# Optimization experiments

Hardware: AMD Instinct MI355X
Metric: run time of the kernel (lower is better)

Reference implementation:

```python
import jax, jax.numpy as jnp
import numpy as np

N, E, D = 50000, 1600000, 128


def _mk_w(key, shape):
    return jax.random.normal(key, shape, dtype=jnp.float32) * 0.05


def setup_inputs() -> dict:
    key = jax.random.key(0)
    ks = jax.random.split(key, 32)
    inp = {
        'x_in': jax.random.normal(ks[0], (N, D), dtype=jnp.float32),
        'rows': jax.random.randint(ks[1], (E,), 0, N, dtype=jnp.int64 if jax.config.jax_enable_x64 else jnp.int32),
        'cols': jax.random.randint(ks[2], (E,), 0, N, dtype=jnp.int64 if jax.config.jax_enable_x64 else jnp.int32),
        'vals': jax.random.uniform(ks[3], (E,), dtype=jnp.float32),
    }
    names = ['m1_W1', 'm1_W2', 'm2_W1', 'm2_W2', 'Wu1', 'Wu2', 'Wr1', 'Wr2', 'Wo1', 'Wo2']
    for i, n in enumerate(names):
        inp[n] = _mk_w(ks[4 + i], (D, D))
        inp[n.replace('W', 'b')] = jnp.zeros((D,), dtype=jnp.float32)
    return inp


def _mlp2(x, W1, b1, W2, b2):
    # 2-layer MLP: Linear -> ReLU -> Linear
    return jax.nn.relu(x @ W1 + b1) @ W2 + b2


def reference(x_in, rows, cols, vals,
              m1_W1, m1_b1, m1_W2, m1_b2,
              m2_W1, m2_b1, m2_W2, m2_b2,
              Wu1, bu1, Wu2, bu2,
              Wr1, br1, Wr2, br2,
              Wo1, bo1, Wo2, bo2):
    x = _mlp2(x_in, m1_W1, m1_b1, m1_W2, m1_b2)            # [N, D]
    # sparse COO spmm: out[i] = sum_e vals[e] * x[cols[e]] for rows[e] == i
    msgs = vals[:, None] * x[cols]                          # [E, D]
    agg = jax.ops.segment_sum(msgs, rows, num_segments=N)   # [N, D]
    out = _mlp2(agg, m2_W1, m2_b1, m2_W2, m2_b2)
    z = jax.nn.sigmoid(out @ Wu1 + bu1 + x @ Wu2 + bu2)
    r = jax.nn.sigmoid(out @ Wr1 + br1 + x @ Wr2 + br2)
    h = jnp.tanh(out @ Wo1 + bo1 + (r * x) @ Wo2 + bo2)
    return (1.0 - z) * x + z * h
```

## Files before the change

### kernel.cpp

```cpp
#include <hip/hip_runtime.h>

#define DD 128
#define BSHIFT 7
#define BROWS 128
#define MS_TILE 4096
#define MS_EPT 8
#define STAGE_CAP 6144

typedef __attribute__((ext_vector_type(8))) short short8;
typedef __attribute__((ext_vector_type(4))) float f32x4;
typedef unsigned short u16;
typedef unsigned int u32;

__device__ __forceinline__ u16 f2bf(float f) {
  u32 u = __builtin_bit_cast(u32, f);
  u += 0x7fffu + ((u >> 16) & 1u);
  return (u16)(u >> 16);
}
__device__ __forceinline__ float bf2f(u16 s) {
  u32 u = ((u32)s) << 16;
  return __builtin_bit_cast(float, u);
}
__device__ __forceinline__ float f16val(u32 cv) {
  return (float)__builtin_bit_cast(_Float16, (u16)(cv & 0xffffu));
}
__device__ __forceinline__ float sigmoidf_(float v) { return 1.f / (1.f + __expf(-v)); }
__device__ __forceinline__ float tanhf_(float v) {
  float e = __expf(-2.f * v);
  return (1.f - e) / (1.f + e);
}

struct WPtrs { const float* w[10]; };

__global__ void pack_weights(WPtrs wp, u16* __restrict__ bp) {
  const float* W = wp.w[blockIdx.x];
  u16* out = bp + (size_t)blockIdx.x * 16384;
  for (int o = threadIdx.x; o < 16384; o += blockDim.x) {
    int e = o & 7, lane = (o >> 3) & 63, nt = (o >> 9) & 7, ks = o >> 12;
    int k = ks * 32 + (lane >> 4) * 8 + e;
    int c = (lane & 15) + nt * 16;
    out[o] = f2bf(W[k * DD + c]);
  }
}

__global__ __launch_bounds__(512) void multisplit(const int* __restrict__ rows,
                                                  const int* __restrict__ cols,
                                                  const float* __restrict__ vals,
                                                  int* __restrict__ cursor,
                                                  uint2* __restrict__ recs,
                                                  int E, int NB, int cap) {
  __shared__ u32 hist[512];
  __shared__ u32 scan_tmp[512];
  __shared__ u32 hbase[512];
  __shared__ int gbase[512];
  __shared__ u32 rankc[512];
  __shared__ uint2 stage[MS_TILE];
  const int t = threadIdx.x;
  const int tile0 = blockIdx.x * MS_TILE;
  hist[t] = 0;
  rankc[t] = 0;
  __syncthreads();
  int myb[MS_EPT];
  u32 mycv[MS_EPT], myrow[MS_EPT];
#pragma unroll
  for (int j = 0; j < MS_EPT; ++j) {
    int e = tile0 + j * 512 + t;
    if (e < E) {
      int r = rows[e];
      int b = r >> BSHIFT;
      myb[j] = b;
      myrow[j] = (u32)r;
      _Float16 hf = (_Float16)vals[e];
      mycv[j] = ((u32)cols[e] << 16) | (u32)__builtin_bit_cast(u16, hf);
      atomicAdd(&hist[b], 1u);
    } else {
      myb[j] = -1;
    }
  }
  __syncthreads();
  u32 v = hist[t];
  scan_tmp[t] = v;
  __syncthreads();
  for (int o = 1; o < 512; o <<= 1) {
    u32 x = (t >= o) ? scan_tmp[t - o] : 0;
    __syncthreads();
    scan_tmp[t] += x;
    __syncthreads();
  }
  hbase[t] = scan_tmp[t] - v;
  if (t < NB && v > 0) gbase[t] = atomicAdd(&cursor[t], (int)v);
  __syncthreads();
#pragma unroll
  for (int j = 0; j < MS_EPT; ++j) {
    if (myb[j] >= 0) {
      u32 rk = atomicAdd(&rankc[myb[j]], 1u);
      stage[hbase[myb[j]] + rk].x = mycv[j];
      stage[hbase[myb[j]] + rk].y = myrow[j];
    }
  }
  __syncthreads();
  int cnt = E - tile0;
  cnt = cnt < MS_TILE ? cnt : MS_TILE;
  for (int k = t; k < cnt; k += 512) {
    uint2 rec = stage[k];
    int b = (int)(rec.y >> BSHIFT);
    int off = gbase[b] + (k - (int)hbase[b]);
    if (off < cap) recs[(size_t)b * cap + off] = rec;
  }
}

__global__ __launch_bounds__(512) void bucket_csr(const uint2* __restrict__ recs,
                                                  const int* __restrict__ cursor,
                                                  u32* __restrict__ recs2,
                                                  int* __restrict__ rowstart,
                                                  int* __restrict__ rowcnt, int n, int cap) {
  __shared__ int hist[BROWS];
  __shared__ int sc[BROWS];
  __shared__ int hbase[BROWS];
  __shared__ u32 rank[BROWS];
  __shared__ u32 stage[STAGE_CAP];
  const int t = threadIdx.x;
  const int b = blockIdx.x;
  int cnt = cursor[b];
  cnt = cnt < cap ? cnt : cap;
  const uint2* rb = recs + (size_t)b * cap;
  if (t < BROWS) { hist[t] = 0; rank[t] = 0; }
  __syncthreads();
  for (int i = t; i < cnt; i += 512) atomicAdd(&hist[rb[i].y & (BROWS - 1)], 1);
  __syncthreads();
  if (t < BROWS) sc[t] = hist[t];
  __syncthreads();
  for (int o = 1; o < BROWS; o <<= 1) {
    int x = (t >= o && t < BROWS) ? sc[t - o] : 0;
    __syncthreads();
    if (t < BROWS) sc[t] += x;
    __syncthreads();
  }
  if (t < BROWS) {
    hbase[t] = sc[t] - hist[t];
    int r = (b << BSHIFT) + t;
    if (r < n) {
      rowstart[r] = b * cap + hbase[t];
      rowcnt[r] = hist[t];
    }
  }
  __syncthreads();
  for (int i = t; i < cnt; i += 512) {
    uint2 rec = rb[i];
    int lr = (int)(rec.y & (BROWS - 1));
    u32 p = atomicAdd(&rank[lr], 1u);
    stage[hbase[lr] + p] = rec.x;
  }
  __syncthreads();
  u32* ob = recs2 + (size_t)b * cap;
  for (int i = t; i < cnt; i += 512) ob[i] = stage[i];
}

__global__ void spmm_agg(const int* __restrict__ rowstart, const int* __restrict__ rowcnt,
                         const u32* __restrict__ recs2, const u16* __restrict__ xb,
                         u16* __restrict__ aggb, int n) {
  int row = blockIdx.x * 4 + (threadIdx.x >> 6);
  int lane = threadIdx.x & 63;
  if (row >= n) return;
  int s = rowstart[row];
  int e2 = s + rowcnt[row];
  float a0 = 0.f, a1 = 0.f;
  int j = s;
  for (; j + 3 < e2; j += 4) {
    u32 pk0 = recs2[j], pk1 = recs2[j + 1], pk2 = recs2[j + 2], pk3 = recs2[j + 3];
    u32 x0 = *reinterpret_cast<const u32*>(xb + (size_t)(pk0 >> 16) * DD + lane * 2);
    u32 x1 = *reinterpret_cast<const u32*>(xb + (size_t)(pk1 >> 16) * DD + lane * 2);
    u32 x2 = *reinterpret_cast<const u32*>(xb + (size_t)(pk2 >> 16) * DD + lane * 2);
    u32 x3 = *reinterpret_cast<const u32*>(xb + (size_t)(pk3 >> 16) * DD + lane * 2);
    float v0 = f16val(pk0), v1 = f16val(pk1), v2 = f16val(pk2), v3 = f16val(pk3);
    a0 += v0 * bf2f((u16)(x0 & 0xffff)) + v1 * bf2f((u16)(x1 & 0xffff)) +
          v2 * bf2f((u16)(x2 & 0xffff)) + v3 * bf2f((u16)(x3 & 0xffff));
    a1 += v0 * bf2f((u16)(x0 >> 16)) + v1 * bf2f((u16)(x1 >> 16)) +
          v2 * bf2f((u16)(x2 >> 16)) + v3 * bf2f((u16)(x3 >> 16));
  }
  for (; j < e2; ++j) {
    u32 pk = recs2[j];
    u32 x0 = *reinterpret_cast<const u32*>(xb + (size_t)(pk >> 16) * DD + lane * 2);
    float v0 = f16val(pk);
    a0 += v0 * bf2f((u16)(x0 & 0xffff));
    a1 += v0 * bf2f((u16)(x0 >> 16));
  }
  u32 o = ((u32)f2bf(a1) << 16) | (u32)f2bf(a0);
  *reinterpret_cast<u32*>(aggb + (size_t)row * DD + lane * 2) = o;
}

template <int ASRC>
__global__ __launch_bounds__(256) void mlp_fused(const void* __restrict__ Ain,
                                                 const u16* __restrict__ W1p,
                                                 const float* __restrict__ b1,
                                                 const u16* __restrict__ W2p,
                                                 const float* __restrict__ b2,
                                                 u16* __restrict__ outB, int n) {
  __shared__ u16 sm[4][32][136];
  const int lane = threadIdx.x & 63;
  const int wid = threadIdx.x >> 6;
  const int row0 = blockIdx.x * 128 + wid * 32;
  const int ar = lane & 15, ak = (lane >> 4) * 8;
  const int crow = 4 * (lane >> 4), ccol = lane & 15;

  f32x4 acc[2][8];
#pragma unroll
  for (int m = 0; m < 2; ++m)
#pragma unroll
    for (int t = 0; t < 8; ++t) acc[m][t] = f32x4{0.f, 0.f, 0.f, 0.f};

#pragma unroll
  for (int ks = 0; ks < 4; ++ks) {
    short8 a[2];
#pragma unroll
    for (int m = 0; m < 2; ++m) {
      int r = row0 + m * 16 + ar;
      r = r < n ? r : n - 1;
      if (ASRC == 0) {
        const float* Ap = (const float*)Ain + (size_t)r * DD + ks * 32 + ak;
        float4 f0 = *reinterpret_cast<const float4*>(Ap);
        float4 f1 = *reinterpret_cast<const float4*>(Ap + 4);
        short8 tv;
        tv[0] = (short)f2bf(f0.x); tv[1] = (short)f2bf(f0.y);
        tv[2] = (short)f2bf(f0.z); tv[3] = (short)f2bf(f0.w);
        tv[4] = (short)f2bf(f1.x); tv[5] = (short)f2bf(f1.y);
        tv[6] = (short)f2bf(f1.z); tv[7] = (short)f2bf(f1.w);
        a[m] = tv;
      } else {
        a[m] = *reinterpret_cast<const short8*>((const u16*)Ain + (size_t)r * DD + ks * 32 + ak);
      }
    }
#pragma unroll
    for (int nt = 0; nt < 8; ++nt) {
      short8 bfr = *reinterpret_cast<const short8*>(W1p + (((ks * 8 + nt) * 64 + lane) * 8));
#pragma unroll
      for (int m = 0; m < 2; ++m)
        acc[m][nt] = __builtin_amdgcn_mfma_f32_16x16x32_bf16(a[m], bfr, acc[m][nt], 0, 0, 0);
    }
  }
#pragma unroll
  for (int m = 0; m < 2; ++m)
#pragma unroll
    for (int nt = 0; nt < 8; ++nt) {
      float bsv = b1[ccol + nt * 16];
#pragma unroll
      for (int e = 0; e < 4; ++e) {
        float v = acc[m][nt][e] + bsv;
        v = v > 0.f ? v : 0.f;
        sm[wid][m * 16 + crow + e][ccol + nt * 16] = f2bf(v);
      }
    }
  __syncthreads();

  f32x4 acc2[2][8];
#pragma unroll
  for (int m = 0; m < 2; ++m)
#pragma unroll
    for (int t = 0; t < 8; ++t) acc2[m][t] = f32x4{0.f, 0.f, 0.f, 0.f};
#pragma unroll
  for (int ks = 0; ks < 4; ++ks) {
    short8 a2[2];
#pragma unroll
    for (int m = 0; m < 2; ++m)
      a2[m] = *reinterpret_cast<const short8*>(&sm[wid][m * 16 + ar][ks * 32 + ak]);
#pragma unroll
    for (int nt = 0; nt < 8; ++nt) {
      short8 bfr = *reinterpret_cast<const short8*>(W2p + (((ks * 8 + nt) * 64 + lane) * 8));
#pragma unroll
      for (int m = 0; m < 2; ++m)
        acc2[m][nt] = __builtin_amdgcn_mfma_f32_16x16x32_bf16(a2[m], bfr, acc2[m][nt], 0, 0, 0);
    }
  }
#pragma unroll
  for (int m = 0; m < 2; ++m)
#pragma unroll
    for (int nt = 0; nt < 8; ++nt) {
      int col = ccol + nt * 16;
      float bsv = b2[col];
#pragma unroll
      for (int e = 0; e < 4; ++e) {
        int r = row0 + m * 16 + crow + e;
        if (r < n) outB[(size_t)r * DD + col] = f2bf(acc2[m][nt][e] + bsv);
      }
    }
}

__global__ __launch_bounds__(256) void gates_final(
    const u16* __restrict__ Ao, const u16* __restrict__ Ax, const u16* __restrict__ Wu1p,
    const u16* __restrict__ Wu2p, const u16* __restrict__ Wr1p, const u16* __restrict__ Wr2p,
    const u16* __restrict__ Wo1p, const u16* __restrict__ Wo2p, const float* __restrict__ bu1,
    const float* __restrict__ bu2, const float* __restrict__ br1, const float* __restrict__ br2,
    const float* __restrict__ bo1, const float* __restrict__ bo2, float* __restrict__ out,
    int n) {
  __shared__ u16 sm[4][16][136];
  const int lane = threadIdx.x & 63;
  const int wid = threadIdx.x >> 6;
  const int row0 = blockIdx.x * 64 + wid * 16;
  const int ar = lane & 15, ak = (lane >> 4) * 8;
  const int crow = 4 * (lane >> 4), ccol = lane & 15;

  f32x4 aZ[8], aR[8], aO[8];
#pragma unroll
  for (int t = 0; t < 8; ++t) {
    aZ[t] = f32x4{0.f, 0.f, 0.f, 0.f};
    aR[t] = f32x4{0.f, 0.f, 0.f, 0.f};
    aO[t] = f32x4{0.f, 0.f, 0.f, 0.f};
  }
#pragma unroll
  for (int ks = 0; ks < 4; ++ks) {
    int r = row0 + ar;
    r = r < n ? r : n - 1;
    short8 ao = *reinterpret_cast<const short8*>(Ao + (size_t)r * DD + ks * 32 + ak);
    short8 ax = *reinterpret_cast<const short8*>(Ax + (size_t)r * DD + ks * 32 + ak);
#pragma unroll
    for (int nt = 0; nt < 8; ++nt) {
      size_t bo = (size_t)(((ks * 8 + nt) * 64 + lane) * 8);
      short8 b1 = *reinterpret_cast<const short8*>(Wu1p + bo);
      short8 b2 = *reinterpret_cast<const short8*>(Wu2p + bo);
      short8 b3 = *reinterpret_cast<const short8*>(Wr1p + bo);
      short8 b4 = *reinterpret_cast<const short8*>(Wr2p + bo);
      short8 b5 = *reinterpret_cast<const short8*>(Wo1p + bo);
      aZ[nt] = __builtin_amdgcn_mfma_f32_16x16x32_bf16(ao, b1, aZ[nt], 0, 0, 0);
      aZ[nt] = __builtin_amdgcn_mfma_f32_16x16x32_bf16(ax, b2, aZ[nt], 0, 0, 0);
      aR[nt] = __builtin_amdgcn_mfma_f32_16x16x32_bf16(ao, b3, aR[nt], 0, 0, 0);
      aR[nt] = __builtin_amdgcn_mfma_f32_16x16x32_bf16(ax, b4, aR[nt], 0, 0, 0);
      aO[nt] = __builtin_amdgcn_mfma_f32_16x16x32_bf16(ao, b5, aO[nt], 0, 0, 0);
    }
  }
#pragma unroll
  for (int nt = 0; nt < 8; ++nt) {
    int col = ccol + nt * 16;
    float bz = bu1[col] + bu2[col];
    float br_ = br1[col] + br2[col];
    float bo_ = bo1[col];
#pragma unroll
    for (int e = 0; e < 4; ++e) {
      int r = row0 + crow + e;
      float z = sigmoidf_(aZ[nt][e] + bz);
      float rr = sigmoidf_(aR[nt][e] + br_);
      aZ[nt][e] = z;
      aO[nt][e] = aO[nt][e] + bo_;
      float xv = 0.f;
      if (r < n) xv = bf2f(Ax[(size_t)r * DD + col]);
      sm[wid][crow + e][col] = f2bf(rr * xv);
    }
  }
  __syncthreads();

  f32x4 acc2[8];
#pragma unroll
  for (int t = 0; t < 8; ++t) acc2[t] = f32x4{0.f, 0.f, 0.f, 0.f};
#pragma unroll
  for (int ks = 0; ks < 4; ++ks) {
    short8 a2 = *reinterpret_cast<const short8*>(&sm[wid][ar][ks * 32 + ak]);
#pragma unroll
    for (int nt = 0; nt < 8; ++nt) {
      short8 bfr = *reinterpret_cast<const short8*>(Wo2p + (((ks * 8 + nt) * 64 + lane) * 8));
      acc2[nt] = __builtin_amdgcn_mfma_f32_16x16x32_bf16(a2, bfr, acc2[nt], 0, 0, 0);
    }
  }
#pragma unroll
  for (int nt = 0; nt < 8; ++nt) {
    int col = ccol + nt * 16;
    float bo2v = bo2[col];
#pragma unroll
    for (int e = 0; e < 4; ++e) {
      int r = row0 + crow + e;
      if (r < n) {
        size_t idx = (size_t)r * DD + col;
        float oi = acc2[nt][e] + bo2v + aO[nt][e];
        float h = tanhf_(oi);
        float z = aZ[nt][e];
        float xv = bf2f(Ax[idx]);
        out[idx] = (1.f - z) * xv + z * h;
      }
    }
  }
}

extern "C" void kernel_launch(void* const* d_in, const int* in_sizes, int n_in,
                              void* d_out, int out_size, void* d_ws, size_t ws_size,
                              hipStream_t stream) {
  const int n = in_sizes[0] / DD;
  const int E = in_sizes[1];
  const float* x_in = (const float*)d_in[0];
  const int* rows = (const int*)d_in[1];
  const int* cols = (const int*)d_in[2];
  const float* vals = (const float*)d_in[3];
  const float* Wm[10];
  const float* Bm[10];
  for (int i = 0; i < 10; ++i) {
    Wm[i] = (const float*)d_in[4 + 2 * i];
    Bm[i] = (const float*)d_in[5 + 2 * i];
  }

  const int NB = (n + BROWS - 1) >> BSHIFT;
  int cap = (((E / NB) * 5) / 4 + 511) & ~511;
  cap = cap < STAGE_CAP ? cap : STAGE_CAP;

  char* base = (char*)d_ws;
  size_t off = 0;
  auto alloc = [&](size_t bytes) -> char* {
    char* p = base + off;
    off += (bytes + 255) & ~(size_t)255;
    return p;
  };
  u16* wpack = (u16*)alloc((size_t)10 * 16384 * 2);
  u16* x_b = (u16*)alloc((size_t)n * DD * 2);
  u16* agg_b = (u16*)alloc((size_t)n * DD * 2);
  int* cursor = (int*)alloc((size_t)NB * 4);
  int* rowstart = (int*)alloc((size_t)n * 4);
  int* rowcnt = (int*)alloc((size_t)n * 4);
  uint2* recs = (uint2*)alloc((size_t)NB * cap * 8);
  u32* recs2 = (u32*)alloc((size_t)NB * cap * 4);
  (void)ws_size;
  (void)n_in;
  (void)out_size;

  hipMemsetAsync(cursor, 0, (size_t)NB * 4, stream);
  WPtrs wp;
  for (int i = 0; i < 10; ++i) wp.w[i] = Wm[i];
  pack_weights<<<10, 256, 0, stream>>>(wp, wpack);
  multisplit<<<(E + MS_TILE - 1) / MS_TILE, 512, 0, stream>>>(rows, cols, vals, cursor, recs, E,
                                                             NB, cap);
  bucket_csr<<<NB, 512, 0, stream>>>(recs, cursor, recs2, rowstart, rowcnt, n, cap);
  int gblocks = (n + 127) / 128;
  mlp_fused<0><<<gblocks, 256, 0, stream>>>(x_in, wpack + 0 * 16384, Bm[0], wpack + 1 * 16384,
                                            Bm[1], x_b, n);
  spmm_agg<<<(n + 3) / 4, 256, 0, stream>>>(rowstart, rowcnt, recs2, x_b, agg_b, n);
  mlp_fused<1><<<gblocks, 256, 0, stream>>>(agg_b, wpack + 2 * 16384, Bm[2], wpack + 3 * 16384,
                                            Bm[3], agg_b, n);
  gates_final<<<(n + 63) / 64, 256, 0, stream>>>(
      agg_b, x_b, wpack + 4 * 16384, wpack + 5 * 16384, wpack + 6 * 16384, wpack + 7 * 16384,
      wpack + 8 * 16384, wpack + 9 * 16384, Bm[4], Bm[5], Bm[6], Bm[7], Bm[8], Bm[9],
      (float*)d_out, n);
}
```

Measured before the change: 357.1 us.

## Split MLP and gate GEMM tiles across waves by row and column halves

Result: faster. 306.1 us (-14.3%).

```diff
diff --git a/kernel.cpp b/kernel.cpp
--- a/kernel.cpp
+++ b/kernel.cpp
@@ -196,93 +196,79 @@
                                                  const u16* __restrict__ W2p,
                                                  const float* __restrict__ b2,
                                                  u16* __restrict__ outB, int n) {
-  __shared__ u16 sm[4][32][136];
+  __shared__ u16 sm[32][136];
   const int lane = threadIdx.x & 63;
   const int wid = threadIdx.x >> 6;
-  const int row0 = blockIdx.x * 128 + wid * 32;
+  const int m = wid >> 1, c = wid & 1;
+  const int row0 = blockIdx.x * 32 + m * 16;
   const int ar = lane & 15, ak = (lane >> 4) * 8;
   const int crow = 4 * (lane >> 4), ccol = lane & 15;
 
-  f32x4 acc[2][8];
-#pragma unroll
-  for (int m = 0; m < 2; ++m)
-#pragma unroll
-    for (int t = 0; t < 8; ++t) acc[m][t] = f32x4{0.f, 0.f, 0.f, 0.f};
+  f32x4 acc[4];
+#pragma unroll
+  for (int t = 0; t < 4; ++t) acc[t] = f32x4{0.f, 0.f, 0.f, 0.f};
 
 #pragma unroll
   for (int ks = 0; ks < 4; ++ks) {
-    short8 a[2];
-#pragma unroll
-    for (int m = 0; m < 2; ++m) {
-      int r = row0 + m * 16 + ar;
-      r = r < n ? r : n - 1;
-      if (ASRC == 0) {
-        const float* Ap = (const float*)Ain + (size_t)r * DD + ks * 32 + ak;
-        float4 f0 = *reinterpret_cast<const float4*>(Ap);
-        float4 f1 = *reinterpret_cast<const float4*>(Ap + 4);
-        short8 tv;
-        tv[0] = (short)f2bf(f0.x); tv[1] = (short)f2bf(f0.y);
-        tv[2] = (short)f2bf(f0.z); tv[3] = (short)f2bf(f0.w);
-        tv[4] = (short)f2bf(f1.x); tv[5] = (short)f2bf(f1.y);
-        tv[6] = (short)f2bf(f1.z); tv[7] = (short)f2bf(f1.w);
-        a[m] = tv;
-      } else {
-        a[m] = *reinterpret_cast<const short8*>((const u16*)Ain + (size_t)r * DD + ks * 32 + ak);
-      }
-    }
-#pragma unroll
-    for (int nt = 0; nt < 8; ++nt) {
+    short8 a;
+    int r = row0 + ar;
+    r = r < n ? r : n - 1;
+    if (ASRC == 0) {
+      const float* Ap = (const float*)Ain + (size_t)r * DD + ks * 32 + ak;
+      float4 f0 = *reinterpret_cast<const float4*>(Ap);
+      float4 f1 = *reinterpret_cast<const float4*>(Ap + 4);
+      short8 tv;
+      tv[0] = (short)f2bf(f0.x); tv[1] = (short)f2bf(f0.y);
+      tv[2] = (short)f2bf(f0.z); tv[3] = (short)f2bf(f0.w);
+      tv[4] = (short)f2bf(f1.x); tv[5] = (short)f2bf(f1.y);
+      tv[6] = (short)f2bf(f1.z); tv[7] = (short)f2bf(f1.w);
+      a = tv;
+    } else {
+      a = *reinterpret_cast<const short8*>((const u16*)Ain + (size_t)r * DD + ks * 32 + ak);
+    }
+#pragma unroll
+    for (int nt4 = 0; nt4 < 4; ++nt4) {
+      int nt = c * 4 + nt4;
       short8 bfr = *reinterpret_cast<const short8*>(W1p + (((ks * 8 + nt) * 64 + lane) * 8));
-#pragma unroll
-      for (int m = 0; m < 2; ++m)
-        acc[m][nt] = __builtin_amdgcn_mfma_f32_16x16x32_bf16(a[m], bfr, acc[m][nt], 0, 0, 0);
-    }
-  }
-#pragma unroll
-  for (int m = 0; m < 2; ++m)
-#pragma unroll
-    for (int nt = 0; nt < 8; ++nt) {
-      float bsv = b1[ccol + nt * 16];
-#pragma unroll
-      for (int e = 0; e < 4; ++e) {
-        float v = acc[m][nt][e] + bsv;
-        v = v > 0.f ? v : 0.f;
-        sm[wid][m * 16 + crow + e][ccol + nt * 16] = f2bf(v);
-      }
-    }
-  __syncthreads();
-
-  f32x4 acc2[2][8];
-#pragma unroll
-  for (int m = 0; m < 2; ++m)
-#pragma unroll
-    for (int t = 0; t < 8; ++t) acc2[m][t] = f32x4{0.f, 0.f, 0.f, 0.f};
+      acc[nt4] = __builtin_amdgcn_mfma_f32_16x16x32_bf16(a, bfr, acc[nt4], 0, 0, 0);
+    }
+  }
+#pragma unroll
+  for (int nt4 = 0; nt4 < 4; ++nt4) {
+    int col = (c * 4 + nt4) * 16 + ccol;
+    float bsv = b1[col];
+#pragma unroll
+    for (int e = 0; e < 4; ++e) {
+      float v = acc[nt4][e] + bsv;
+      v = v > 0.f ? v : 0.f;
+      sm[m * 16 + crow + e][col] = f2bf(v);
+    }
+  }
+  __syncthreads();
+
+  f32x4 acc2[4];
+#pragma unroll
+  for (int t = 0; t < 4; ++t) acc2[t] = f32x4{0.f, 0.f, 0.f, 0.f};
 #pragma unroll
   for (int ks = 0; ks < 4; ++ks) {
-    short8 a2[2];
-#pragma unroll
-    for (int m = 0; m < 2; ++m)
-      a2[m] = *reinterpret_cast<const short8*>(&sm[wid][m * 16 + ar][ks * 32 + ak]);
-#pragma unroll
-    for (int nt = 0; nt < 8; ++nt) {
+    short8 a2 = *reinterpret_cast<const short8*>(&sm[m * 16 + ar][ks * 32 + ak]);
+#pragma unroll
+    for (int nt4 = 0; nt4 < 4; ++nt4) {
+      int nt = c * 4 + nt4;
       short8 bfr = *reinterpret_cast<const short8*>(W2p + (((ks * 8 + nt) * 64 + lane) * 8));
-#pragma unroll
-      for (int m = 0; m < 2; ++m)
-        acc2[m][nt] = __builtin_amdgcn_mfma_f32_16x16x32_bf16(a2[m], bfr, acc2[m][nt], 0, 0, 0);
-    }
-  }
-#pragma unroll
-  for (int m = 0; m < 2; ++m)
-#pragma unroll
-    for (int nt = 0; nt < 8; ++nt) {
-      int col = ccol + nt * 16;
-      float bsv = b2[col];
-#pragma unroll
-      for (int e = 0; e < 4; ++e) {
-        int r = row0 + m * 16 + crow + e;
-        if (r < n) outB[(size_t)r * DD + col] = f2bf(acc2[m][nt][e] + bsv);
-      }
-    }
+      acc2[nt4] = __builtin_amdgcn_mfma_f32_16x16x32_bf16(a2, bfr, acc2[nt4], 0, 0, 0);
+    }
+  }
+#pragma unroll
+  for (int nt4 = 0; nt4 < 4; ++nt4) {
+    int col = (c * 4 + nt4) * 16 + ccol;
+    float bsv = b2[col];
+#pragma unroll
+    for (int e = 0; e < 4; ++e) {
+      int r = row0 + crow + e;
+      if (r < n) outB[(size_t)r * DD + col] = f2bf(acc2[nt4][e] + bsv);
+    }
+  }
 }
 
 __global__ __launch_bounds__(256) void gates_final(
@@ -292,16 +278,17 @@
     const float* __restrict__ bu2, const float* __restrict__ br1, const float* __restrict__ br2,
     const float* __restrict__ bo1, const float* __restrict__ bo2, float* __restrict__ out,
     int n) {
-  __shared__ u16 sm[4][16][136];
+  __shared__ u16 sm[32][136];
   const int lane = threadIdx.x & 63;
   const int wid = threadIdx.x >> 6;
-  const int row0 = blockIdx.x * 64 + wid * 16;
+  const int m = wid >> 1, c = wid & 1;
+  const int row0 = blockIdx.x * 32 + m * 16;
   const int ar = lane & 15, ak = (lane >> 4) * 8;
   const int crow = 4 * (lane >> 4), ccol = lane & 15;
 
-  f32x4 aZ[8], aR[8], aO[8];
-#pragma unroll
-  for (int t = 0; t < 8; ++t) {
+  f32x4 aZ[4], aR[4], aO[4];
+#pragma unroll
+  for (int t = 0; t < 4; ++t) {
     aZ[t] = f32x4{0.f, 0.f, 0.f, 0.f};
     aR[t] = f32x4{0.f, 0.f, 0.f, 0.f};
     aO[t] = f32x4{0.f, 0.f, 0.f, 0.f};
@@ -313,64 +300,66 @@
     short8 ao = *reinterpret_cast<const short8*>(Ao + (size_t)r * DD + ks * 32 + ak);
     short8 ax = *reinterpret_cast<const short8*>(Ax + (size_t)r * DD + ks * 32 + ak);
 #pragma unroll
-    for (int nt = 0; nt < 8; ++nt) {
+    for (int nt4 = 0; nt4 < 4; ++nt4) {
+      int nt = c * 4 + nt4;
       size_t bo = (size_t)(((ks * 8 + nt) * 64 + lane) * 8);
       short8 b1 = *reinterpret_cast<const short8*>(Wu1p + bo);
       short8 b2 = *reinterpret_cast<const short8*>(Wu2p + bo);
       short8 b3 = *reinterpret_cast<const short8*>(Wr1p + bo);
       short8 b4 = *reinterpret_cast<const short8*>(Wr2p + bo);
       short8 b5 = *reinterpret_cast<const short8*>(Wo1p + bo);
-      aZ[nt] = __builtin_amdgcn_mfma_f32_16x16x32_bf16(ao, b1, aZ[nt], 0, 0, 0);
-      aZ[nt] = __builtin_amdgcn_mfma_f32_16x16x32_bf16(ax, b2, aZ[nt], 0, 0, 0);
-      aR[nt] = __builtin_amdgcn_mfma_f32_16x16x32_bf16(ao, b3, aR[nt], 0, 0, 0);
-      aR[nt] = __builtin_amdgcn_mfma_f32_16x16x32_bf16(ax, b4, aR[nt], 0, 0, 0);
-      aO[nt] = __builtin_amdgcn_mfma_f32_16x16x32_bf16(ao, b5, aO[nt], 0, 0, 0);
-    }
-  }
-#pragma unroll
-  for (int nt = 0; nt < 8; ++nt) {
-    int col = ccol + nt * 16;
+      aZ[nt4] = __builtin_amdgcn_mfma_f32_16x16x32_bf16(ao, b1, aZ[nt4], 0, 0, 0);
+      aZ[nt4] = __builtin_amdgcn_mfma_f32_16x16x32_bf16(ax, b2, aZ[nt4], 0, 0, 0);
+      aR[nt4] = __builtin_amdgcn_mfma_f32_16x16x32_bf16(ao, b3, aR[nt4], 0, 0, 0);
+      aR[nt4] = __builtin_amdgcn_mfma_f32_16x16x32_bf16(ax, b4, aR[nt4], 0, 0, 0);
+      aO[nt4] = __builtin_amdgcn_mfma_f32_16x16x32_bf16(ao, b5, aO[nt4], 0, 0, 0);
+    }
+  }
+#pragma unroll
+  for (int nt4 = 0; nt4 < 4; ++nt4) {
+    int col = (c * 4 + nt4) * 16 + ccol;
     float bz = bu1[col] + bu2[col];
     float br_ = br1[col] + br2[col];
     float bo_ = bo1[col];
 #pragma unroll
     for (int e = 0; e < 4; ++e) {
       int r = row0 + crow + e;
-      float z = sigmoidf_(aZ[nt][e] + bz);
-      float rr = sigmoidf_(aR[nt][e] + br_);
-      aZ[nt][e] = z;
-      aO[nt][e] = aO[nt][e] + bo_;
+      float z = sigmoidf_(aZ[nt4][e] + bz);
+      float rr = sigmoidf_(aR[nt4][e] + br_);
+      aZ[nt4][e] = z;
+      aO[nt4][e] = aO[nt4][e] + bo_;
       float xv = 0.f;
       if (r < n) xv = bf2f(Ax[(size_t)r * DD + col]);
-      sm[wid][crow + e][col] = f2bf(rr * xv);
-    }
-  }
-  __syncthreads();
-
-  f32x4 acc2[8];
-#pragma unroll
-  for (int t = 0; t < 8; ++t) acc2[t] = f32x4{0.f, 0.f, 0.f, 0.f};
+      sm[m * 16 + crow + e][col] = f2bf(rr * xv);
+    }
+  }
+  __syncthreads();
+
+  f32x4 acc2[4];
+#pragma unroll
+  for (int t = 0; t < 4; ++t) acc2[t] = f32x4{0.f, 0.f, 0.f, 0.f};
 #pragma unroll
   for (int ks = 0; ks < 4; ++ks) {
-    short8 a2 = *reinterpret_cast<const short8*>(&sm[wid][ar][ks * 32 + ak]);
-#pragma unroll
-    for (int nt = 0; nt < 8; ++nt) {
+    short8 a2 = *reinterpret_cast<const short8*>(&sm[m * 16 + ar][ks * 32 + ak]);
+#pragma unroll
+    for (int nt4 = 0; nt4 < 4; ++nt4) {
+      int nt = c * 4 + nt4;
       short8 bfr = *reinterpret_cast<const short8*>(Wo2p + (((ks * 8 + nt) * 64 + lane) * 8));
-      acc2[nt] = __builtin_amdgcn_mfma_f32_16x16x32_bf16(a2, bfr, acc2[nt], 0, 0, 0);
-    }
-  }
-#pragma unroll
-  for (int nt = 0; nt < 8; ++nt) {
-    int col = ccol + nt * 16;
+      acc2[nt4] = __builtin_amdgcn_mfma_f32_16x16x32_bf16(a2, bfr, acc2[nt4], 0, 0, 0);
+    }
+  }
+#pragma unroll
+  for (int nt4 = 0; nt4 < 4; ++nt4) {
+    int col = (c * 4 + nt4) * 16 + ccol;
     float bo2v = bo2[col];
 #pragma unroll
     for (int e = 0; e < 4; ++e) {
       int r = row0 + crow + e;
       if (r < n) {
         size_t idx = (size_t)r * DD + col;
-        float oi = acc2[nt][e] + bo2v + aO[nt][e];
+        float oi = acc2[nt4][e] + bo2v + aO[nt4][e];
         float h = tanhf_(oi);
-        float z = aZ[nt][e];
+        float z = aZ[nt4][e];
         float xv = bf2f(Ax[idx]);
         out[idx] = (1.f - z) * xv + z * h;
       }
@@ -424,13 +413,13 @@
   multisplit<<<(E + MS_TILE - 1) / MS_TILE, 512, 0, stream>>>(rows, cols, vals, cursor, recs, E,
                                                              NB, cap);
   bucket_csr<<<NB, 512, 0, stream>>>(recs, cursor, recs2, rowstart, rowcnt, n, cap);
-  int gblocks = (n + 127) / 128;
+  int gblocks = (n + 31) / 32;
   mlp_fused<0><<<gblocks, 256, 0, stream>>>(x_in, wpack + 0 * 16384, Bm[0], wpack + 1 * 16384,
                                             Bm[1], x_b, n);
   spmm_agg<<<(n + 3) / 4, 256, 0, stream>>>(rowstart, rowcnt, recs2, x_b, agg_b, n);
   mlp_fused<1><<<gblocks, 256, 0, stream>>>(agg_b, wpack + 2 * 16384, Bm[2], wpack + 3 * 16384,
                                             Bm[3], agg_b, n);
-  gates_final<<<(n + 63) / 64, 256, 0, stream>>>(
+  gates_final<<<gblocks, 256, 0, stream>>>(
       agg_b, x_b, wpack + 4 * 16384, wpack + 5 * 16384, wpack + 6 * 16384, wpack + 7 * 16384,
       wpack + 8 * 16384, wpack + 9 * 16384, Bm[4], Bm[5], Bm[6], Bm[7], Bm[8], Bm[9],
       (float*)d_out, n);
```
